# Kernel optimization log

Hardware: AMD Instinct MI355X
Metric: run time of the kernel (lower is better)

## Reference

```python
import jax, jax.numpy as jnp
import numpy as np

VEC_DIM = 128   # D (also the per-head dim in this module)
HEADS = 8
PATCH = 4
WIN = 7
N_BATCH = 4
H_IMG = 448
W_IMG = 448


def _relative_index():
    # Swin-style relative position index, computed statically (matches torch code
    # which uses torch.meshgrid with default 'ij' indexing).
    coords = np.stack(np.meshgrid(np.arange(WIN), np.arange(WIN), indexing='ij'))  # [2,W,W]
    flat = coords.reshape(2, -1)                      # [2, W*W]
    rel = flat[:, :, None] - flat[:, None, :]         # [2, p, p]
    rel = rel.transpose(1, 2, 0).astype(np.int64)     # [p, p, 2]
    rel[:, :, 0] += WIN - 1
    rel[:, :, 1] += WIN - 1
    rel[:, :, 1] *= 2 * WIN - 1
    return rel.sum(-1)                                # [p, p], values in [0, (2W-1)^2)

REL_IDX = jnp.asarray(_relative_index())


def setup_inputs() -> dict:
    key = jax.random.key(0)
    ks = jax.random.split(key, 8)
    P = (H_IMG // PATCH) * (W_IMG // PATCH)  # 12544
    D, H = VEC_DIM, HEADS
    s = 0.02
    return {
        'x': jax.random.normal(ks[0], (N_BATCH, D, P), jnp.float32),
        'Wq': jax.random.normal(ks[1], (H * D, D), jnp.float32) * s,
        'bq': jnp.zeros((H * D,), jnp.float32),
        'Wk': jax.random.normal(ks[2], (H * D, D), jnp.float32) * s,
        'bk': jnp.zeros((H * D,), jnp.float32),
        'Wv': jax.random.normal(ks[3], (H * D, D), jnp.float32) * s,
        'bv': jnp.zeros((H * D,), jnp.float32),
        'Wo': jax.random.normal(ks[4], (D, H * D), jnp.float32) * s,
        'bo': jnp.zeros((D,), jnp.float32),
        'pos_code': jax.random.normal(ks[5], ((2 * WIN - 1) ** 2, H), jnp.float32) * s,
        'h': H_IMG,
        'w': W_IMG,
    }


def reference(x, Wq, bq, Wk, bk, Wv, bv, Wo, bo, pos_code, h, w):
    N, D, P = x.shape
    H = HEADS
    ch, cw = h // PATCH, w // PATCH
    nh, nw = ch // WIN, cw // WIN            # windows per axis
    p = WIN * WIN                            # tokens per window

    def emb(W, b):
        # pointwise Conv1d: [N,D,P] -> [N,H*D,P] -> [N,H,D,P]
        return (jnp.einsum('od,ndp->nop', W, x) + b[None, :, None]).reshape(N, H, D, P)

    def partition(e):
        # [N,H,D,P] -> [N,H,win_num,D,p]
        e = e.reshape(N, H, D, nh, WIN, nw, WIN)
        return e.transpose(0, 1, 3, 5, 2, 4, 6).reshape(N, H, nh * nw, D, p)

    q = partition(emb(Wq, bq))
    k = partition(emb(Wk, bk))
    v = partition(emb(Wv, bv))

    # attn[n,h,w,i,j] = sum_d k[n,h,w,d,i] * q[n,h,w,d,j], scaled
    attn = jnp.einsum('nhwdi,nhwdj->nhwij', k, q) / (D ** 0.5)
    bias = pos_code[REL_IDX].transpose(2, 0, 1)          # [H, p, p]
    attn = attn + bias[None, :, None, :, :]
    weights = jax.nn.softmax(attn, axis=3)               # softmax over key index i

    # out[n,h,w,d,j] = sum_i v[n,h,w,d,i] * weights[n,h,w,i,j]
    out = jnp.einsum('nhwdi,nhwij->nhwdj', v, weights)

    # window merge: [N,H,win_num,D,p] -> [N,H*D,P]
    out = out.reshape(N, H, nh, nw, D, WIN, WIN)
    out = out.transpose(0, 1, 4, 2, 5, 3, 6).reshape(N, H * D, P)

    return jnp.einsum('od,ndp->nop', Wo, out) + bo[None, :, None]
```

## Files before the change

kernel.cpp:

```cpp
#include <hip/hip_runtime.h>
#include <hip/hip_bf16.h>

typedef unsigned short u16;
typedef unsigned int u32;
typedef __attribute__((ext_vector_type(8))) short bf16x8;
typedef __attribute__((ext_vector_type(4))) float f32x4;
typedef __attribute__((ext_vector_type(2))) unsigned int u32x2;

#define NBATCH 4
#define DDIM   128
#define NHEAD  8
#define PTOT   12544
#define CWID   112
#define NTOK   49
#define PSTR   68
#define SCALE  0.08838834764831845f

#define BUFSZ   16384
#define OFF_US  8192
#define OFF_PL  32768
#define OFF_PCF 36100
#define OFF_CS  38804
#define LDS_TOT 39828

__device__ __forceinline__ float bf2f(u16 u) {
    union { u32 i; float f; } x; x.i = ((u32)u) << 16; return x.f;
}
__device__ __forceinline__ u16 f2bf(float f) {
    union { float f; u32 u; } v; v.f = f;
    return (u16)((v.u + 0x7fffu + ((v.u >> 16) & 1u)) >> 16);
}
__device__ __forceinline__ u32 pk2(float a, float b) {
    union { __hip_bfloat162 h; u32 u; } c;
    float2 t; t.x = a; t.y = b;
    c.h = __float22bfloat162_rn(t);
    return c.u;
}
__device__ __forceinline__ int swz128(int row, int col) {
    return row * 128 + ((((col >> 3) ^ (row & 15)) & 15) << 3) + (col & 7);
}

#define WS_WC   131072
#define WS_F32  262144

__global__ void __launch_bounds__(256) prep(
    const float* __restrict__ Wq, const float* __restrict__ Wk,
    const float* __restrict__ Wv, const float* __restrict__ Wo,
    const float* __restrict__ bq, const float* __restrict__ bk,
    const float* __restrict__ bv, u16* __restrict__ ws)
{
    __shared__ u16 lm[18432];
    const int tid = threadIdx.x;
    const int bb  = blockIdx.x;
    const int b   = bb >> 3;
    const int sub = bb & 7;
    const bool isG = (b >= 8);
    const int h = b & 7;
    const int r0 = sub * 16;
    float* fb = (float*)(ws + WS_F32);

    if (!isG) {
        for (int idx = tid; idx < 2048; idx += 256) {
            const int lr = idx >> 7, dh = idx & 127;
            lm[swz128(lr, dh)] = f2bf(Wo[(r0 + lr) * 1024 + h * 128 + dh]);
        }
        for (int idx = tid; idx < 16384; idx += 256) {
            const int dh = idx >> 7, d = idx & 127;
            lm[2048 + swz128(d, dh)] = f2bf(Wv[(h * 128 + dh) * 128 + d]);
        }
        if (sub == 0 && tid < 128) {
            float s = 0.f;
            for (int dh = 0; dh < 128; ++dh)
                s += Wo[tid * 1024 + h * 128 + dh] * bv[h * 128 + dh];
            fb[h * 128 + tid] = s;
        }
    } else {
        for (int idx = tid; idx < 2048; idx += 256) {
            const int dh = idx >> 4, lr = idx & 15;
            lm[swz128(lr, dh)] = f2bf(Wk[(h * 128 + dh) * 128 + r0 + lr]);
        }
        for (int idx = tid; idx < 16384; idx += 256) {
            const int dh = idx >> 7, dp = idx & 127;
            lm[2048 + swz128(dp, dh)] = f2bf(Wq[(h * 128 + dh) * 128 + dp]);
        }
        if (sub == 0 && tid < 128) {
            float r = 0.f, m = 0.f;
            for (int dh = 0; dh < 128; ++dh) {
                r += bk[h * 128 + dh] * Wq[(h * 128 + dh) * 128 + tid];
                m += Wk[(h * 128 + dh) * 128 + tid] * bq[h * 128 + dh];
            }
            fb[1024 + h * 128 + tid] = r * SCALE;
            fb[2048 + h * 128 + tid] = m * SCALE;
        }
        if (sub == 0 && tid == 0) {
            float s = 0.f;
            for (int dh = 0; dh < 128; ++dh) s += bk[h * 128 + dh] * bq[h * 128 + dh];
            fb[3072 + h] = s * SCALE;
        }
    }
    __syncthreads();

    const int w = tid >> 6, lane = tid & 63, quad = lane >> 4, lid = lane & 15;
    const f32x4 z4 = {0.f, 0.f, 0.f, 0.f};
    u16* dst = ws + (isG ? 0 : WS_WC) + h * 16384;
    const float gs = isG ? SCALE : 1.0f;
    bf16x8 A[4];
    #pragma unroll
    for (int kt = 0; kt < 4; ++kt)
        A[kt] = *(const bf16x8*)(lm + swz128(lid, kt * 32 + quad * 8));
    #pragma unroll
    for (int ntl = 0; ntl < 2; ++ntl) {
        const int nt = 2 * w + ntl;
        f32x4 acc = z4;
        #pragma unroll
        for (int kt = 0; kt < 4; ++kt) {
            bf16x8 B = *(const bf16x8*)(lm + 2048 + swz128(nt * 16 + lid, kt * 32 + quad * 8));
            acc = __builtin_amdgcn_mfma_f32_16x16x32_bf16(A[kt], B, acc, 0, 0, 0);
        }
        #pragma unroll
        for (int r = 0; r < 4; ++r) {
            const int row = r0 + quad * 4 + r, col = nt * 16 + lid;
            if (isG) dst[col * 128 + row] = f2bf(acc[r] * gs);
            else     dst[row * 128 + col] = f2bf(acc[r]);
        }
    }
}

#define STAGE_B(WW) \
    _Pragma("unroll") \
    for (int mt = 0; mt < 4; ++mt) { \
        _Pragma("unroll") \
        for (int kt = 0; kt < 4; ++kt) { \
            bf16x8 Abf = *(const bf16x8*)(tsb + (mt * 16 + lid) * 128 + ((((kt * 4 + quad) ^ lid) & 15) << 3)); \
            S[mt] = __builtin_amdgcn_mfma_f32_16x16x32_bf16(Abf, xfrag[WW][kt], S[mt], 0, 0, 0); \
        } \
    }

__global__ void __launch_bounds__(256, 2)
winattn(const float* __restrict__ xg, const u16* __restrict__ ws,
        const float* __restrict__ bo, const float* __restrict__ posf,
        float* __restrict__ out)
{
    __shared__ __align__(16) u16 sm[LDS_TOT];
    u16* xw  = sm;
    u16* pl  = sm + OFF_PL;
    float* pcf = (float*)(sm + OFF_PCF);
    float* cs  = (float*)(sm + OFF_CS);

    const int tid  = threadIdx.x;
    const int w    = tid >> 6;
    const int lane = tid & 63;
    const int quad = lane >> 4;
    const int lid  = lane & 15;
    const int bx0  = blockIdx.x;
    const int xcd  = bx0 & 7;
    const int idx0 = bx0 >> 3;
    const int n    = idx0 >> 5;
    const int win  = xcd * 32 + (idx0 & 31);
    const int pbase = (win >> 4) * 7 * CWID + (win & 15) * 7;

    const bf16x8 zf = {0,0,0,0,0,0,0,0};
    const f32x4  z4 = {0.f,0.f,0.f,0.f};

    const u16* Gt  = ws;
    const u16* Wcw = ws + WS_WC;
    const float* fb  = (const float*)(ws + WS_F32);
    const float* bcv = fb;
    const float* rP  = fb + 1024;
    const float* MP  = fb + 2048;
    const float* sP  = fb + 3072;

    for (int i = tid; i < 169 * NHEAD; i += 256) pcf[i] = posf[i];
    const float* xn = xg + n * DDIM * PTOT;
    for (int idx = tid; idx < DDIM * NTOK; idx += 256) {
        int d = idx / NTOK;
        int t = idx - d * NTOK;
        int a = t / 7, b = t - a * 7;
        xw[swz128(t, d)] = f2bf(xn[d * PTOT + pbase + a * CWID + b]);
    }
    __syncthreads();

    bf16x8 xfrag[4][4];
    #pragma unroll
    for (int mt = 0; mt < 4; ++mt)
        #pragma unroll
        for (int kt = 0; kt < 4; ++kt)
            xfrag[mt][kt] = (mt * 16 + lid < NTOK)
                ? *(const bf16x8*)(xw + swz128(mt * 16 + lid, kt * 32 + quad * 8)) : zf;
    const int j = 16 * w + lid;

    bf16x8 GA[2][4], WBn[2][4];
    #pragma unroll
    for (int mtl = 0; mtl < 2; ++mtl)
        #pragma unroll
        for (int kt = 0; kt < 4; ++kt) {
            GA[mtl][kt]  = *(const bf16x8*)(Gt  + ((2 * w + mtl) * 16 + lid) * 128 + kt * 32 + quad * 8);
            WBn[mtl][kt] = *(const bf16x8*)(Wcw + ((2 * w + mtl) * 16 + lid) * 128 + kt * 32 + quad * 8);
        }

    for (int hh = w; hh < NHEAD; hh += 4) {
        const float sh = sP[hh];
        #pragma unroll
        for (int mt = 0; mt < 4; ++mt) {
            float c = 0.f;
            #pragma unroll
            for (int kt = 0; kt < 4; ++kt)
                #pragma unroll
                for (int jj = 0; jj < 8; ++jj)
                    c += bf2f((u16)xfrag[mt][kt][jj]) * MP[hh * 128 + kt * 32 + quad * 8 + jj];
            c += __shfl_xor(c, 16);
            c += __shfl_xor(c, 32);
            if (quad == 0) cs[hh * 64 + mt * 16 + lid] = c + sh;
        }
    }
    __syncthreads();

    f32x4 outacc[8];
    #pragma unroll
    for (int nt = 0; nt < 8; ++nt) outacc[nt] = z4;

    const int jc = j < NTOK ? j : NTOK - 1;
    const int aj = jc / 7, bj = jc - aj * 7;

    #pragma unroll 2
    for (int h = 0; h < NHEAD; ++h) {
        u16* tsb = sm + (h & 1) * BUFSZ;
        u16* usb = tsb + OFF_US;

        __builtin_amdgcn_s_setprio(1);
        #pragma unroll
        for (int mtl = 0; mtl < 2; ++mtl) {
            const int mt = 2 * w + mtl;
            const f32x4 rb = *(const f32x4*)(rP + h * 128 + mt * 16 + quad * 4);
            const int dpb = mt * 16 + quad * 4;
            #pragma unroll
            for (int nt = 0; nt < 4; ++nt) {
                f32x4 acc = z4;
                #pragma unroll
                for (int kt = 0; kt < 4; ++kt)
                    acc = __builtin_amdgcn_mfma_f32_16x16x32_bf16(GA[mtl][kt], xfrag[nt][kt], acc, 0, 0, 0);
                const int i = nt * 16 + lid;
                u32x2 pkv;
                pkv.x = pk2(acc[0] + rb[0], acc[1] + rb[1]);
                pkv.y = pk2(acc[2] + rb[2], acc[3] + rb[3]);
                *(u32x2*)(tsb + i * 128 + ((((dpb >> 3) ^ (i & 15)) & 15) << 3) + (dpb & 7)) = pkv;
            }
        }
        #pragma unroll
        for (int ntl = 0; ntl < 2; ++ntl) {
            const int nt = 2 * w + ntl;
            const int dd = nt * 16 + lid;
            const float bb = bcv[h * 128 + dd];
            #pragma unroll
            for (int mt = 0; mt < 4; ++mt) {
                f32x4 acc = z4;
                #pragma unroll
                for (int kt = 0; kt < 4; ++kt)
                    acc = __builtin_amdgcn_mfma_f32_16x16x32_bf16(xfrag[mt][kt], WBn[ntl][kt], acc, 0, 0, 0);
                const int ib = mt * 16 + quad * 4;
                u32x2 pkv;
                pkv.x = pk2(acc[0] + bb, acc[1] + bb);
                pkv.y = pk2(acc[2] + bb, acc[3] + bb);
                *(u32x2*)(usb + dd * 64 + ((((ib >> 3) ^ (dd & 7)) & 7) << 3) + (ib & 7)) = pkv;
            }
        }
        __builtin_amdgcn_s_setprio(0);

        {
            const int hn = (h + 1) & 7;
            #pragma unroll
            for (int mtl = 0; mtl < 2; ++mtl)
                #pragma unroll
                for (int kt = 0; kt < 4; ++kt)
                    GA[mtl][kt] = *(const bf16x8*)(Gt + hn * 16384 + ((2 * w + mtl) * 16 + lid) * 128 + kt * 32 + quad * 8);
        }

        asm volatile("s_waitcnt lgkmcnt(0)" ::: "memory");
        __builtin_amdgcn_s_barrier();
        asm volatile("" ::: "memory");

        f32x4 S[4];
        #pragma unroll
        for (int mt = 0; mt < 4; ++mt) S[mt] = z4;
        __builtin_amdgcn_s_setprio(1);
        if      (w == 0) { STAGE_B(0) }
        else if (w == 1) { STAGE_B(1) }
        else if (w == 2) { STAGE_B(2) }
        else             { STAGE_B(3) }
        __builtin_amdgcn_s_setprio(0);

        float sv[4][4];
        float ssum = 0.f;
        #pragma unroll
        for (int mt = 0; mt < 4; ++mt) {
            const f32x4 csv = *(const f32x4*)(cs + h * 64 + mt * 16 + quad * 4);
            #pragma unroll
            for (int r = 0; r < 4; ++r) {
                const int ii = mt * 16 + quad * 4 + r;
                float e;
                if (ii < NTOK) {
                    const int ai = ii / 7, bi = ii - ai * 7;
                    const int rel = (ai - aj + 6) + 13 * (bi - bj + 6);
                    e = __expf(S[mt][r] + csv[r] + pcf[rel * NHEAD + h]);
                } else {
                    e = 0.0f;
                }
                sv[mt][r] = e;
                ssum += e;
            }
        }
        ssum += __shfl_xor(ssum, 16);
        ssum += __shfl_xor(ssum, 32);
        const float inv = __builtin_amdgcn_rcpf(ssum);
        if (j < NTOK) {
            #pragma unroll
            for (int mt = 0; mt < 4; ++mt) {
                u32x2 pkv;
                pkv.x = pk2(sv[mt][0] * inv, sv[mt][1] * inv);
                pkv.y = pk2(sv[mt][2] * inv, sv[mt][3] * inv);
                *(u32x2*)(pl + j * PSTR + mt * 16 + quad * 4) = pkv;
            }
        }

        {
            const int hn = (h + 1) & 7;
            #pragma unroll
            for (int ntl = 0; ntl < 2; ++ntl)
                #pragma unroll
                for (int kt = 0; kt < 4; ++kt)
                    WBn[ntl][kt] = *(const bf16x8*)(Wcw + hn * 16384 + ((2 * w + ntl) * 16 + lid) * 128 + kt * 32 + quad * 8);
        }

        asm volatile("s_waitcnt lgkmcnt(0)" ::: "memory");

        __builtin_amdgcn_s_setprio(1);
        #pragma unroll
        for (int kt = 0; kt < 2; ++kt) {
            union { bf16x8 v; u32 u[4]; } Af;
            #pragma unroll
            for (int q2 = 0; q2 < 4; ++q2)
                Af.u[q2] = *(const u32*)(pl + jc * PSTR + kt * 32 + quad * 8 + 2 * q2);
            #pragma unroll
            for (int nt = 0; nt < 8; ++nt) {
                const int dd = nt * 16 + lid;
                bf16x8 Bu = *(const bf16x8*)(usb + dd * 64 + ((((kt * 4 + quad) ^ (dd & 7)) & 7) << 3));
                outacc[nt] = __builtin_amdgcn_mfma_f32_16x16x32_bf16(Af.v, Bu, outacc[nt], 0, 0, 0);
            }
        }
        __builtin_amdgcn_s_setprio(0);
    }

    float* outp = out + n * DDIM * PTOT;
    #pragma unroll
    for (int nt = 0; nt < 8; ++nt) {
        const int dd = nt * 16 + lid;
        const float bov = bo[dd];
        #pragma unroll
        for (int r = 0; r < 4; ++r) {
            const int jj = 16 * w + quad * 4 + r;
            if (jj < NTOK) {
                const int a = jj / 7, b = jj - a * 7;
                outp[dd * PTOT + pbase + a * CWID + b] = outacc[nt][r] + bov;
            }
        }
    }
}

extern "C" void kernel_launch(void* const* d_in, const int* in_sizes, int n_in,
                              void* d_out, int out_size, void* d_ws, size_t ws_size,
                              hipStream_t stream) {
    (void)in_sizes; (void)n_in; (void)ws_size; (void)out_size;
    prep<<<128, 256, 0, stream>>>((const float*)d_in[1], (const float*)d_in[3],
                                  (const float*)d_in[5], (const float*)d_in[7],
                                  (const float*)d_in[2], (const float*)d_in[4],
                                  (const float*)d_in[6], (u16*)d_ws);
    winattn<<<NBATCH * 256, 256, 0, stream>>>(
        (const float*)d_in[0], (const u16*)d_ws,
        (const float*)d_in[8], (const float*)d_in[9], (float*)d_out);
}
```

Baseline: 220.5 us.

## Software-pipeline next head's projection into double buffer before PV stage

Hoists the head-0 T/U projection out of the loop, then computes head h+1's projections into the other LDS buffer after the softmax and before the PV MFMA stage of head h. The goal is to overlap projection MFMAs with the softmax/PV latency and remove one stage from the per-head critical path. WBn register prefetch is replaced by loading Wcw fragments inside the U stage, which cuts persistent register pressure but adds global-load latency inside the stage. Correctness relies on the double-buffered LDS and the existing barrier ordering.

```diff
diff --git a/kernel.cpp b/kernel.cpp
--- a/kernel.cpp
+++ b/kernel.cpp
@@ -136,6 +136,50 @@
         } \
     }
 
+#define STAGE_A_T(HH, TSB) \
+    _Pragma("unroll") \
+    for (int mtl = 0; mtl < 2; ++mtl) { \
+        const int mt_ = 2 * w + mtl; \
+        const f32x4 rb_ = *(const f32x4*)(rP + (HH) * 128 + mt_ * 16 + quad * 4); \
+        const int dpb_ = mt_ * 16 + quad * 4; \
+        _Pragma("unroll") \
+        for (int nt = 0; nt < 4; ++nt) { \
+            f32x4 acc_ = z4; \
+            _Pragma("unroll") \
+            for (int kt = 0; kt < 4; ++kt) \
+                acc_ = __builtin_amdgcn_mfma_f32_16x16x32_bf16(GA[mtl][kt], xfrag[nt][kt], acc_, 0, 0, 0); \
+            const int i_ = nt * 16 + lid; \
+            u32x2 pkv_; \
+            pkv_.x = pk2(acc_[0] + rb_[0], acc_[1] + rb_[1]); \
+            pkv_.y = pk2(acc_[2] + rb_[2], acc_[3] + rb_[3]); \
+            *(u32x2*)((TSB) + i_ * 128 + ((((dpb_ >> 3) ^ (i_ & 15)) & 15) << 3) + (dpb_ & 7)) = pkv_; \
+        } \
+    }
+
+#define STAGE_A_U(HH, USB) \
+    _Pragma("unroll") \
+    for (int ntl = 0; ntl < 2; ++ntl) { \
+        const int nt_ = 2 * w + ntl; \
+        bf16x8 Bw[4]; \
+        _Pragma("unroll") \
+        for (int kt = 0; kt < 4; ++kt) \
+            Bw[kt] = *(const bf16x8*)(Wcw + (HH) * 16384 + (nt_ * 16 + lid) * 128 + kt * 32 + quad * 8); \
+        const int dd_ = nt_ * 16 + lid; \
+        const float bb_ = bcv[(HH) * 128 + dd_]; \
+        _Pragma("unroll") \
+        for (int mt = 0; mt < 4; ++mt) { \
+            f32x4 acc_ = z4; \
+            _Pragma("unroll") \
+            for (int kt = 0; kt < 4; ++kt) \
+                acc_ = __builtin_amdgcn_mfma_f32_16x16x32_bf16(xfrag[mt][kt], Bw[kt], acc_, 0, 0, 0); \
+            const int ib_ = mt * 16 + quad * 4; \
+            u32x2 pkv_; \
+            pkv_.x = pk2(acc_[0] + bb_, acc_[1] + bb_); \
+            pkv_.y = pk2(acc_[2] + bb_, acc_[3] + bb_); \
+            *(u32x2*)((USB) + dd_ * 64 + ((((ib_ >> 3) ^ (dd_ & 7)) & 7) << 3) + (ib_ & 7)) = pkv_; \
+        } \
+    }
+
 __global__ void __launch_bounds__(256, 2)
 winattn(const float* __restrict__ xg, const u16* __restrict__ ws,
         const float* __restrict__ bo, const float* __restrict__ posf,
@@ -189,14 +233,12 @@
                 ? *(const bf16x8*)(xw + swz128(mt * 16 + lid, kt * 32 + quad * 8)) : zf;
     const int j = 16 * w + lid;
 
-    bf16x8 GA[2][4], WBn[2][4];
+    bf16x8 GA[2][4];
     #pragma unroll
     for (int mtl = 0; mtl < 2; ++mtl)
         #pragma unroll
-        for (int kt = 0; kt < 4; ++kt) {
-            GA[mtl][kt]  = *(const bf16x8*)(Gt  + ((2 * w + mtl) * 16 + lid) * 128 + kt * 32 + quad * 8);
-            WBn[mtl][kt] = *(const bf16x8*)(Wcw + ((2 * w + mtl) * 16 + lid) * 128 + kt * 32 + quad * 8);
-        }
+        for (int kt = 0; kt < 4; ++kt)
+            GA[mtl][kt] = *(const bf16x8*)(Gt + ((2 * w + mtl) * 16 + lid) * 128 + kt * 32 + quad * 8);
 
     for (int hh = w; hh < NHEAD; hh += 4) {
         const float sh = sP[hh];
@@ -222,52 +264,20 @@
     const int jc = j < NTOK ? j : NTOK - 1;
     const int aj = jc / 7, bj = jc - aj * 7;
 
+    __builtin_amdgcn_s_setprio(1);
+    STAGE_A_T(0, sm)
+    STAGE_A_U(0, sm + OFF_US)
+    __builtin_amdgcn_s_setprio(0);
+
     #pragma unroll 2
     for (int h = 0; h < NHEAD; ++h) {
         u16* tsb = sm + (h & 1) * BUFSZ;
         u16* usb = tsb + OFF_US;
-
-        __builtin_amdgcn_s_setprio(1);
-        #pragma unroll
-        for (int mtl = 0; mtl < 2; ++mtl) {
-            const int mt = 2 * w + mtl;
-            const f32x4 rb = *(const f32x4*)(rP + h * 128 + mt * 16 + quad * 4);
-            const int dpb = mt * 16 + quad * 4;
-            #pragma unroll
-            for (int nt = 0; nt < 4; ++nt) {
-                f32x4 acc = z4;
-                #pragma unroll
-                for (int kt = 0; kt < 4; ++kt)
-                    acc = __builtin_amdgcn_mfma_f32_16x16x32_bf16(GA[mtl][kt], xfrag[nt][kt], acc, 0, 0, 0);
-                const int i = nt * 16 + lid;
-                u32x2 pkv;
-                pkv.x = pk2(acc[0] + rb[0], acc[1] + rb[1]);
-                pkv.y = pk2(acc[2] + rb[2], acc[3] + rb[3]);
-                *(u32x2*)(tsb + i * 128 + ((((dpb >> 3) ^ (i & 15)) & 15) << 3) + (dpb & 7)) = pkv;
-            }
-        }
-        #pragma unroll
-        for (int ntl = 0; ntl < 2; ++ntl) {
-            const int nt = 2 * w + ntl;
-            const int dd = nt * 16 + lid;
-            const float bb = bcv[h * 128 + dd];
-            #pragma unroll
-            for (int mt = 0; mt < 4; ++mt) {
-                f32x4 acc = z4;
-                #pragma unroll
-                for (int kt = 0; kt < 4; ++kt)
-                    acc = __builtin_amdgcn_mfma_f32_16x16x32_bf16(xfrag[mt][kt], WBn[ntl][kt], acc, 0, 0, 0);
-                const int ib = mt * 16 + quad * 4;
-                u32x2 pkv;
-                pkv.x = pk2(acc[0] + bb, acc[1] + bb);
-                pkv.y = pk2(acc[2] + bb, acc[3] + bb);
-                *(u32x2*)(usb + dd * 64 + ((((ib >> 3) ^ (dd & 7)) & 7) << 3) + (ib & 7)) = pkv;
-            }
-        }
-        __builtin_amdgcn_s_setprio(0);
-
-        {
-            const int hn = (h + 1) & 7;
+        u16* tsb2 = sm + ((h + 1) & 1) * BUFSZ;
+        u16* usb2 = tsb2 + OFF_US;
+
+        if (h < NHEAD - 1) {
+            const int hn = h + 1;
             #pragma unroll
             for (int mtl = 0; mtl < 2; ++mtl)
                 #pragma unroll
@@ -321,17 +331,14 @@
                 *(u32x2*)(pl + j * PSTR + mt * 16 + quad * 4) = pkv;
             }
         }
-
-        {
-            const int hn = (h + 1) & 7;
-            #pragma unroll
-            for (int ntl = 0; ntl < 2; ++ntl)
-                #pragma unroll
-                for (int kt = 0; kt < 4; ++kt)
-                    WBn[ntl][kt] = *(const bf16x8*)(Wcw + hn * 16384 + ((2 * w + ntl) * 16 + lid) * 128 + kt * 32 + quad * 8);
-        }
-
         asm volatile("s_waitcnt lgkmcnt(0)" ::: "memory");
+
+        if (h < NHEAD - 1) {
+            __builtin_amdgcn_s_setprio(1);
+            STAGE_A_T(h + 1, tsb2)
+            STAGE_A_U(h + 1, usb2)
+            __builtin_amdgcn_s_setprio(0);
+        }
 
         __builtin_amdgcn_s_setprio(1);
         #pragma unroll
```

Measured after the change: 211.2 us. 1.04x faster.
